# Optimization experiments

Measured on AMD Instinct MI355X. Metric: run time of the kernel, lower is better.

## Reference

```python
import math
import jax, jax.numpy as jnp
import numpy as np

D_MODEL = 1024
N_HEADS = 16
D_HEAD = D_MODEL // N_HEADS
ROPE_BASE = 10000.0
MAX_SEQ_LEN = 2048


def build_cos_sin_cache(d_head, max_seq_len, base=ROPE_BASE):
    half = d_head // 2
    i = jnp.arange(half, dtype=jnp.float32)
    theta = 1.0 / (base ** (2.0 * i / d_head))  # (half,)
    t = jnp.arange(max_seq_len, dtype=jnp.float32)
    angles = jnp.outer(t, theta)  # (T, half)
    return jnp.cos(angles), jnp.sin(angles)


def rotate_half(x):
    d = x.shape[-1]
    x1, x2 = x[..., : d // 2], x[..., d // 2 :]
    return jnp.concatenate([-x2, x1], axis=-1)


def apply_rope(x, cos_t, sin_t):
    # x: (..., T, d_head); cos_t/sin_t: (T, d_head//2)
    cos_full = jnp.concatenate([cos_t, cos_t], axis=-1)
    sin_full = jnp.concatenate([sin_t, sin_t], axis=-1)
    return x * cos_full + rotate_half(x) * sin_full


def setup_inputs() -> dict:
    key = jax.random.key(0)
    ks = jax.random.split(key, 5)
    B, T = 2, 2048
    s = 1.0 / math.sqrt(D_MODEL)
    return {
        "x": jax.random.normal(ks[0], (B, T, D_MODEL), dtype=jnp.float32),
        "Wq": jax.random.normal(ks[1], (D_MODEL, D_MODEL), dtype=jnp.float32) * s,
        "Wk": jax.random.normal(ks[2], (D_MODEL, D_MODEL), dtype=jnp.float32) * s,
        "Wv": jax.random.normal(ks[3], (D_MODEL, D_MODEL), dtype=jnp.float32) * s,
        "Wo": jax.random.normal(ks[4], (D_MODEL, D_MODEL), dtype=jnp.float32) * s,
    }


def reference(x, Wq, Wk, Wv, Wo):
    B, T, _ = x.shape
    # Linear with torch weight convention: y = x @ W.T
    q = jnp.einsum("btd,ed->bte", x, Wq)
    k = jnp.einsum("btd,ed->bte", x, Wk)
    v = jnp.einsum("btd,ed->bte", x, Wv)
    # (B, H, T, d_head)
    q = q.reshape(B, T, N_HEADS, D_HEAD).transpose(0, 2, 1, 3)
    k = k.reshape(B, T, N_HEADS, D_HEAD).transpose(0, 2, 1, 3)
    v = v.reshape(B, T, N_HEADS, D_HEAD).transpose(0, 2, 1, 3)
    cos_c, sin_c = build_cos_sin_cache(D_HEAD, MAX_SEQ_LEN)
    cos_t, sin_t = cos_c[:T], sin_c[:T]
    q = apply_rope(q, cos_t, sin_t)
    k = apply_rope(k, cos_t, sin_t)
    scale = math.sqrt(D_HEAD)
    scores = jnp.einsum("bhqd,bhkd->bhqk", q, k) / scale
    causal = jnp.triu(jnp.full((T, T), -jnp.inf, dtype=x.dtype), k=1)
    scores = scores + causal
    weights = jax.nn.softmax(scores, axis=-1)
    out = jnp.einsum("bhqk,bhkd->bhqd", weights, v)
    out = out.transpose(0, 2, 1, 3).reshape(B, T, D_MODEL)
    return jnp.einsum("btd,ed->bte", out, Wo)
```

## Files before the change

kernel.cpp:

```cpp
#include <hip/hip_runtime.h>
#include <stdint.h>
#include <math.h>

typedef __attribute__((ext_vector_type(8))) short short8;
typedef __attribute__((ext_vector_type(4))) float f32x4;
typedef __attribute__((ext_vector_type(16))) float f32x16;

#define T_SEQ 2048
#define MROWS 4096
#define LOG2E 1.44269504088896f

#define OFF_XBF   ((size_t)0)
#define OFF_WQ    ((size_t)8388608)
#define OFF_WK    ((size_t)10485760)
#define OFF_WV    ((size_t)12582912)
#define OFF_WO    ((size_t)14680064)
#define OFF_Q     ((size_t)16777216)
#define OFF_K     ((size_t)25165824)
#define OFF_VT    ((size_t)33554432)
#define OFF_ATT   ((size_t)41943040)
#define OFF_COS   ((size_t)50331648)
#define OFF_SIN   ((size_t)50593792)

__device__ __forceinline__ unsigned short f2bf(float f) {
  unsigned u = __float_as_uint(f);
  u += 0x7fffu + ((u >> 16) & 1u);
  return (unsigned short)(u >> 16);
}

__device__ __forceinline__ void gld_lds16(const void* g, void* l) {
  __builtin_amdgcn_global_load_lds(
      (__attribute__((address_space(1))) void*)(g),
      (__attribute__((address_space(3))) void*)(l), 16, 0, 0);
}

__device__ __forceinline__ unsigned cvt_pk_bf16(float lo, float hi) {
  unsigned r;
  asm("v_cvt_pk_bf16_f32 %0, %1, %2" : "=v"(r) : "v"(lo), "v"(hi));
  return r;
}

__global__ void prep_kernel(const float* x, const float* wq, const float* wk,
                            const float* wv, const float* wo, char* ws) {
  const size_t NX4 = (size_t)MROWS * 1024 / 4;
  const size_t NW4 = (size_t)1024 * 1024 / 4;
  const size_t NT = (size_t)T_SEQ * 32;
  unsigned short* xb = (unsigned short*)(ws + OFF_XBF);
  unsigned short* wqb = (unsigned short*)(ws + OFF_WQ);
  unsigned short* wkb = (unsigned short*)(ws + OFF_WK);
  unsigned short* wvb = (unsigned short*)(ws + OFF_WV);
  unsigned short* wob = (unsigned short*)(ws + OFF_WO);
  float* cosb = (float*)(ws + OFF_COS);
  float* sinb = (float*)(ws + OFF_SIN);
  size_t nvec = NX4 + 4 * NW4;
  size_t total = nvec + NT;
  for (size_t i = (size_t)blockIdx.x * blockDim.x + threadIdx.x; i < total;
       i += (size_t)gridDim.x * blockDim.x) {
    if (i < nvec) {
      const float* src;
      unsigned short* dst;
      size_t e;
      if (i < NX4) {
        src = x; dst = xb; e = i * 4;
      } else {
        size_t j = i - NX4;
        int wsel = (int)(j / NW4);
        e = (j - (size_t)wsel * NW4) * 4;
        src = wsel == 0 ? wq : wsel == 1 ? wk : wsel == 2 ? wv : wo;
        dst = wsel == 0 ? wqb : wsel == 1 ? wkb : wsel == 2 ? wvb : wob;
      }
      float4 v = *(const float4*)(src + e);
      unsigned long long p =
          (unsigned long long)f2bf(v.x) |
          ((unsigned long long)f2bf(v.y) << 16) |
          ((unsigned long long)f2bf(v.z) << 32) |
          ((unsigned long long)f2bf(v.w) << 48);
      *(unsigned long long*)(dst + e) = p;
    } else {
      size_t j = i - nvec;
      int t = (int)(j >> 5), ii = (int)(j & 31);
      double th = exp(-(double)ii * (9.210340371976184 / 32.0));
      float ang = (float)t * (float)th;
      cosb[j] = cosf(ang);
      sinb[j] = sinf(ang);
    }
  }
}

__global__ __launch_bounds__(256, 3) void gemm_qkv(
    const unsigned short* Abf, const unsigned short* Wall, unsigned short* qkout,
    unsigned short* vtout, const float* cosT, const float* sinT) {
  const int K = 1024;
  int bid0 = blockIdx.x;
  int bid = (bid0 & 7) * 96 + (bid0 >> 3);
  int bm = bid / 24, bn = bid % 24;
  int sel = bn >> 3, bnc = bn & 7;
  int tid = threadIdx.x;
  int l = tid & 63, w = tid >> 6;
  int wm = w >> 1, wn = w & 1;
  int g = l >> 4;

  __shared__ __align__(16) char ldsbuf[32768];

  auto stage = [&](int kt, int buf) {
    int base = buf * 16384;
#pragma unroll
    for (int i = 0; i < 2; ++i) {
      int p = (w * 2 + i) * 1024;
      int row = (p >> 6) + (l >> 2);
      int u = l & 3;
      const char* ga = (const char*)Abf +
          ((size_t)(bm * 128 + row) * K + (size_t)kt * 32) * 2 + u * 16;
      gld_lds16(ga, ldsbuf + base + p);
      const char* gb = (const char*)Wall +
          ((size_t)(bn * 128 + row) * K + (size_t)kt * 32) * 2 + u * 16;
      gld_lds16(gb, ldsbuf + base + 8192 + p);
    }
  };

  f32x4 acc[4][4] = {};
  stage(0, 0);
  const int nk = K / 32;
  for (int kt = 0; kt < nk; ++kt) {
    int buf = kt & 1;
    if (kt + 1 < nk) {
      stage(kt + 1, buf ^ 1);
      asm volatile("s_waitcnt vmcnt(4)" ::: "memory");
    } else {
      asm volatile("s_waitcnt vmcnt(0)" ::: "memory");
    }
    __builtin_amdgcn_s_barrier();
    __builtin_amdgcn_sched_barrier(0);
    const char* Ab = ldsbuf + buf * 16384;
    const char* Bb = Ab + 8192;
    short8 af[4], bfr[4];
#pragma unroll
    for (int m = 0; m < 4; ++m)
      af[m] = *(const short8*)(Ab + (wm * 64 + m * 16 + (l & 15)) * 64 + g * 16);
#pragma unroll
    for (int n = 0; n < 4; ++n)
      bfr[n] = *(const short8*)(Bb + (wn * 64 + n * 16 + (l & 15)) * 64 + g * 16);
#pragma unroll
    for (int m = 0; m < 4; ++m)
#pragma unroll
      for (int n = 0; n < 4; ++n)
        acc[m][n] = __builtin_amdgcn_mfma_f32_16x16x32_bf16(af[m], bfr[n],
                                                            acc[m][n], 0, 0, 0);
    __builtin_amdgcn_s_barrier();
  }

  int row0 = bm * 128 + wm * 64;
  int col0 = bnc * 128 + wn * 64;
  if (sel < 2) {
    float qscale = sel == 0 ? 0.125f * LOG2E : 1.0f;
    unsigned short* C = qkout + (size_t)sel * MROWS * 1024;
#pragma unroll
    for (int m = 0; m < 4; ++m)
#pragma unroll
      for (int n = 0; n < 2; ++n)
#pragma unroll
        for (int r = 0; r < 4; ++r) {
          int row = row0 + m * 16 + g * 4 + r;
          int t = row & (T_SEQ - 1);
          int d = n * 16 + (l & 15);
          float c = cosT[t * 32 + d], s = sinT[t * 32 + d];
          float v0 = acc[m][n][r], v1 = acc[m][n + 2][r];
          C[(size_t)row * 1024 + col0 + d] = f2bf((v0 * c - v1 * s) * qscale);
          C[(size_t)row * 1024 + col0 + d + 32] = f2bf((v1 * c + v0 * s) * qscale);
        }
  } else {
    unsigned short* C = vtout;
#pragma unroll
    for (int m = 0; m < 4; ++m) {
      int rowb = row0 + m * 16 + g * 4;
      int bb = rowb >> 11, t0 = rowb & (T_SEQ - 1);
#pragma unroll
      for (int n = 0; n < 4; ++n) {
        int e = col0 + n * 16 + (l & 15);
        unsigned long long pv =
            (unsigned long long)f2bf(acc[m][n][0]) |
            ((unsigned long long)f2bf(acc[m][n][1]) << 16) |
            ((unsigned long long)f2bf(acc[m][n][2]) << 32) |
            ((unsigned long long)f2bf(acc[m][n][3]) << 48);
        *(unsigned long long*)(C + ((size_t)bb * 1024 + e) * T_SEQ + t0) = pv;
      }
    }
  }
}

__global__ __launch_bounds__(256, 3) void gemm_wo(const unsigned short* Abf,
                                                  const unsigned short* Wbf,
                                                  float* out) {
  const int K = 1024, N = 1024;
  int bid0 = blockIdx.x;
  int bid = (bid0 & 7) * 64 + (bid0 >> 3);
  int bm = bid >> 4, bn = bid & 15;
  int tid = threadIdx.x;
  int l = tid & 63, w = tid >> 6;
  int wm = w >> 1, wn = w & 1;
  int g = l >> 4;

  __shared__ __align__(16) char ldsbuf[24576];

  auto stage = [&](int kt, int buf) {
    char* base = ldsbuf + buf * 12288;
#pragma unroll
    for (int i = 0; i < 2; ++i) {
      int pos = tid + i * 256;
      int row = pos >> 2, u = pos & 3;
      const char* ga = (const char*)Abf +
          ((size_t)(bm * 128 + row) * K + (size_t)kt * 32) * 2 + u * 16;
      gld_lds16(ga, base + row * 64 + u * 16);
    }
    {
      int row = tid >> 2, u = tid & 3;
      const char* gb = (const char*)Wbf +
          ((size_t)(bn * 64 + row) * K + (size_t)kt * 32) * 2 + u * 16;
      gld_lds16(gb, base + 8192 + row * 64 + u * 16);
    }
  };

  f32x4 acc[4][2] = {};
  stage(0, 0);
  const int nk = K / 32;
  for (int kt = 0; kt < nk; ++kt) {
    int buf = kt & 1;
    if (kt + 1 < nk) {
      stage(kt + 1, buf ^ 1);
      asm volatile("s_waitcnt vmcnt(3)" ::: "memory");
    } else {
      asm volatile("s_waitcnt vmcnt(0)" ::: "memory");
    }
    __builtin_amdgcn_s_barrier();
    __builtin_amdgcn_sched_barrier(0);
    const char* Ab = ldsbuf + buf * 12288;
    const char* Bb = Ab + 8192;
    short8 af[4], bfr[2];
#pragma unroll
    for (int m = 0; m < 4; ++m)
      af[m] = *(const short8*)(Ab + (wm * 64 + m * 16 + (l & 15)) * 64 + g * 16);
#pragma unroll
    for (int n = 0; n < 2; ++n)
      bfr[n] = *(const short8*)(Bb + (wn * 32 + n * 16 + (l & 15)) * 64 + g * 16);
#pragma unroll
    for (int m = 0; m < 4; ++m)
#pragma unroll
      for (int n = 0; n < 2; ++n)
        acc[m][n] = __builtin_amdgcn_mfma_f32_16x16x32_bf16(af[m], bfr[n],
                                                            acc[m][n], 0, 0, 0);
    __builtin_amdgcn_s_barrier();
  }

  int row0 = bm * 128 + wm * 64;
  int col0 = bn * 64 + wn * 32;
#pragma unroll
  for (int m = 0; m < 4; ++m)
#pragma unroll
    for (int n = 0; n < 2; ++n)
#pragma unroll
      for (int r = 0; r < 4; ++r)
        out[(size_t)(row0 + m * 16 + g * 4 + r) * N + col0 + n * 16 + (l & 15)] =
            acc[m][n][r];
}

__global__ __launch_bounds__(256, 2) void attn_kernel(
    const unsigned short* Qbf, const unsigned short* Kbf,
    const unsigned short* VT, unsigned short* att) {
  int bid = blockIdx.x;
  int bh = bid & 31;
  int idx = bid >> 5;
  int qt = idx < 8 ? (15 - idx) : (idx - 8);
  int b = bh >> 4, h = bh & 15;
  int ntt = 2 * qt + 2;
  int hp = ntt >> 1;

  int tid = threadIdx.x;
  int pr = tid >> 7;
  int t127 = tid & 127;
  int l = tid & 63, wv = (tid >> 6) & 1;
  int q32 = l & 31, hi = l >> 5;
  int q0 = qt * 128;
  int q0w = q0 + wv * 64;
  int myKt0 = pr ? hp : 0;
  int ntw = ((q0w + 63) >> 6) + 1 - myKt0;
  if (ntw > hp) ntw = hp;
  if (ntw < 0) ntw = 0;

  __shared__ __align__(16) char lds[2][2][16384];

  short8 qfA[4], qfB[4];
  {
    const char* qb = (const char*)Qbf +
        ((size_t)(b * T_SEQ + q0w + q32)) * 2048 + h * 128 + hi * 16;
#pragma unroll
    for (int ks = 0; ks < 4; ++ks) {
      qfA[ks] = *(const short8*)(qb + ks * 32);
      qfB[ks] = *(const short8*)(qb + 32 * 2048 + ks * 32);
    }
  }
  asm volatile("s_waitcnt vmcnt(0)" ::: "memory");

  auto stage = [&](int gt, int buf) {
    char* Kd = &lds[pr][buf][0];
    char* Vd = &lds[pr][buf][8192];
    int colb = (t127 & 7) * 16;
#pragma unroll
    for (int r = 0; r < 4; ++r) {
      int d = (t127 >> 3) + r * 16;
      int sc = colb ^ ((d & 7) << 4);
      const char* gk = (const char*)Kbf +
          ((size_t)(b * T_SEQ + gt * 64 + d)) * 2048 + h * 128 + sc;
      gld_lds16(gk, Kd + d * 128 + colb);
      const char* gv = (const char*)VT +
          ((size_t)(b * 1024 + h * 64 + d)) * 4096 + gt * 128 + sc;
      gld_lds16(gv, Vd + d * 128 + colb);
    }
  };

  f32x16 oA0 = {}, oA1 = {}, oB0 = {}, oB1 = {};
  float lA = 0.f, lB = 0.f;
  stage(myKt0, 0);
  for (int it = 0; it < hp; ++it) {
    int buf = it & 1;
    if (it + 1 < hp) {
      stage(myKt0 + it + 1, buf ^ 1);
      asm volatile("s_waitcnt vmcnt(8)" ::: "memory");
    } else {
      asm volatile("s_waitcnt vmcnt(0)" ::: "memory");
    }
    __builtin_amdgcn_s_barrier();
    __builtin_amdgcn_sched_barrier(0);
    if (it < ntw) {
      int gt = myKt0 + it;
      const char* Kl = &lds[pr][buf][0];
      const char* Vl = &lds[pr][buf][8192];

      f32x16 sA0 = {}, sA1 = {}, sB0 = {}, sB1 = {};
      __builtin_amdgcn_s_setprio(1);
#pragma unroll
      for (int ks = 0; ks < 4; ++ks) {
        int sc = (ks * 32 + hi * 16) ^ ((q32 & 7) << 4);
        short8 k0 = *(const short8*)(Kl + q32 * 128 + sc);
        short8 k1 = *(const short8*)(Kl + (q32 + 32) * 128 + sc);
        sA0 = __builtin_amdgcn_mfma_f32_32x32x16_bf16(k0, qfA[ks], sA0, 0, 0, 0);
        sA1 = __builtin_amdgcn_mfma_f32_32x32x16_bf16(k1, qfA[ks], sA1, 0, 0, 0);
        sB0 = __builtin_amdgcn_mfma_f32_32x32x16_bf16(k0, qfB[ks], sB0, 0, 0, 0);
        sB1 = __builtin_amdgcn_mfma_f32_32x32x16_bf16(k1, qfB[ks], sB1, 0, 0, 0);
      }
      __builtin_amdgcn_s_setprio(0);

      if (gt * 64 + 63 > q0w) {
        int qA = q0w + q32, qB = qA + 32;
#pragma unroll
        for (int r = 0; r < 16; ++r) {
          int kkb = gt * 64 + (r & 3) + 8 * (r >> 2) + 4 * hi;
          if (kkb > qA) sA0[r] = -1e30f;
          if (kkb + 32 > qA) sA1[r] = -1e30f;
          if (kkb > qB) sB0[r] = -1e30f;
          if (kkb + 32 > qB) sB1[r] = -1e30f;
        }
      }

      float lsA = 0.f, lsB = 0.f;
#pragma unroll
      for (int r = 0; r < 16; ++r) {
        sA0[r] = __builtin_amdgcn_exp2f(sA0[r]);
        sA1[r] = __builtin_amdgcn_exp2f(sA1[r]);
        sB0[r] = __builtin_amdgcn_exp2f(sB0[r]);
        sB1[r] = __builtin_amdgcn_exp2f(sB1[r]);
        lsA += sA0[r] + sA1[r];
        lsB += sB0[r] + sB1[r];
      }
      lA += lsA;
      lB += lsB;

      short8 pbA[4], pbB[4];
#pragma unroll
      for (int ks = 0; ks < 4; ++ks) {
        union { unsigned u[4]; short8 s8; } ua, ub;
#pragma unroll
        for (int j = 0; j < 4; ++j) {
          int bse = (ks & 1) * 8 + 2 * j;
          float a0 = (ks & 2) ? sA1[bse] : sA0[bse];
          float a1 = (ks & 2) ? sA1[bse + 1] : sA0[bse + 1];
          ua.u[j] = cvt_pk_bf16(a0, a1);
          float b0 = (ks & 2) ? sB1[bse] : sB0[bse];
          float b1 = (ks & 2) ? sB1[bse + 1] : sB0[bse + 1];
          ub.u[j] = cvt_pk_bf16(b0, b1);
        }
        pbA[ks] = ua.s8;
        pbB[ks] = ub.s8;
      }

      __builtin_amdgcn_s_setprio(1);
#pragma unroll
      for (int ks = 0; ks < 4; ++ks) {
        int sp = (q32 & 7) << 4;
        int cA = (ks * 32 + 8 * hi) ^ sp;
        int cB = (ks * 32 + 16 + 8 * hi) ^ sp;
#pragma unroll
        for (int cc = 0; cc < 2; ++cc) {
          int dv = cc * 32 + q32;
          union { unsigned long long u[2]; short8 s8; } vv;
          vv.u[0] = *(const unsigned long long*)(Vl + dv * 128 + cA);
          vv.u[1] = *(const unsigned long long*)(Vl + dv * 128 + cB);
          if (cc == 0) {
            oA0 = __builtin_amdgcn_mfma_f32_32x32x16_bf16(vv.s8, pbA[ks], oA0, 0, 0, 0);
            oB0 = __builtin_amdgcn_mfma_f32_32x32x16_bf16(vv.s8, pbB[ks], oB0, 0, 0, 0);
          } else {
            oA1 = __builtin_amdgcn_mfma_f32_32x32x16_bf16(vv.s8, pbA[ks], oA1, 0, 0, 0);
            oB1 = __builtin_amdgcn_mfma_f32_32x32x16_bf16(vv.s8, pbB[ks], oB1, 0, 0, 0);
          }
        }
      }
      __builtin_amdgcn_s_setprio(0);
    }
    __builtin_amdgcn_s_barrier();
  }

  lA += __shfl_xor(lA, 32);
  lB += __shfl_xor(lB, 32);

  float* M = (float*)(&lds[1][0][0]);
  float* Ll = (float*)(&lds[0][0][0]);
  __syncthreads();
  if (pr == 1) {
#pragma unroll
    for (int grp = 0; grp < 2; ++grp)
#pragma unroll
      for (int cc = 0; cc < 2; ++cc)
#pragma unroll
        for (int r = 0; r < 16; ++r) {
          int d = cc * 32 + (r & 3) + 8 * (r >> 2) + 4 * hi;
          float v = grp == 0 ? (cc ? oA1[r] : oA0[r]) : (cc ? oB1[r] : oB0[r]);
          M[(wv * 2 + grp) * 2048 + q32 * 64 + (d ^ (q32 & 31))] = v;
        }
    if (hi == 0) {
      Ll[wv * 128 + q32] = lA;
      Ll[wv * 128 + 64 + q32] = lB;
    }
  }
  __syncthreads();
  if (pr == 0) {
#pragma unroll
    for (int grp = 0; grp < 2; ++grp)
#pragma unroll
      for (int cc = 0; cc < 2; ++cc)
#pragma unroll
        for (int r = 0; r < 16; ++r) {
          int d = cc * 32 + (r & 3) + 8 * (r >> 2) + 4 * hi;
          float v = M[(wv * 2 + grp) * 2048 + q32 * 64 + (d ^ (q32 & 31))];
          if (grp == 0) { if (cc) oA1[r] += v; else oA0[r] += v; }
          else          { if (cc) oB1[r] += v; else oB0[r] += v; }
        }
    lA += Ll[wv * 128 + q32];
    lB += Ll[wv * 128 + 64 + q32];
  }
  __syncthreads();

  float* Ol = (float*)(&lds[0][0][0]);
  if (pr == 0) {
    float scA = 1.0f / lA;
    float scB = 1.0f / lB;
#pragma unroll
    for (int grp = 0; grp < 2; ++grp)
#pragma unroll
      for (int cc = 0; cc < 2; ++cc)
#pragma unroll
        for (int r = 0; r < 16; ++r) {
          int d = cc * 32 + (r & 3) + 8 * (r >> 2) + 4 * hi;
          float v;
          if (grp == 0) v = (cc ? oA1[r] : oA0[r]) * scA;
          else          v = (cc ? oB1[r] : oB0[r]) * scB;
          Ol[(wv * 2 + grp) * 2048 + q32 * 64 + (d ^ (q32 & 31))] = v;
        }
  }
  __syncthreads();

#pragma unroll
  for (int i = 0; i < 4; ++i) {
    int idx2 = tid + i * 256;
    int row = idx2 >> 3;
    int seg = idx2 & 7;
    int q = row & 31, rg = row >> 5;
    unsigned short tmp[8];
#pragma unroll
    for (int j = 0; j < 8; ++j) {
      int d = seg * 8 + j;
      tmp[j] = f2bf(Ol[rg * 2048 + q * 64 + (d ^ (q & 31))]);
    }
    *(unsigned long long*)(att + ((size_t)(b * T_SEQ + q0 + row)) * 1024 +
                           h * 64 + seg * 8) = *(unsigned long long*)&tmp[0];
    *(unsigned long long*)(att + ((size_t)(b * T_SEQ + q0 + row)) * 1024 +
                           h * 64 + seg * 8 + 4) = *(unsigned long long*)&tmp[4];
  }
}

extern "C" void kernel_launch(void* const* d_in, const int* in_sizes, int n_in,
                              void* d_out, int out_size, void* d_ws,
                              size_t ws_size, hipStream_t stream) {
  const float* x = (const float*)d_in[0];
  const float* Wq = (const float*)d_in[1];
  const float* Wk = (const float*)d_in[2];
  const float* Wv = (const float*)d_in[3];
  const float* Wo = (const float*)d_in[4];
  char* ws = (char*)d_ws;

  unsigned short* xb = (unsigned short*)(ws + OFF_XBF);
  unsigned short* wall = (unsigned short*)(ws + OFF_WQ);
  unsigned short* wob = (unsigned short*)(ws + OFF_WO);
  unsigned short* qbf = (unsigned short*)(ws + OFF_Q);
  unsigned short* vtb = (unsigned short*)(ws + OFF_VT);
  unsigned short* att = (unsigned short*)(ws + OFF_ATT);
  unsigned short* kbf = (unsigned short*)(ws + OFF_K);
  const float* cosT = (const float*)(ws + OFF_COS);
  const float* sinT = (const float*)(ws + OFF_SIN);

  prep_kernel<<<2048, 256, 0, stream>>>(x, Wq, Wk, Wv, Wo, ws);
  gemm_qkv<<<768, 256, 0, stream>>>(xb, wall, qbf, vtb, cosT, sinT);
  attn_kernel<<<512, 256, 0, stream>>>(qbf, kbf, vtb, att);
  gemm_wo<<<512, 256, 0, stream>>>(att, wob, (float*)d_out);
}
```

Baseline: 99.42 us.

## Double QKV GEMM K-tile to 64 with XOR-swizzled LDS layout

The QKV projection GEMM now stages 64-wide K slices per iteration instead of 32, which halves the number of barrier-synchronised main-loop iterations and doubles the LDS buffers to 64KB. It also applies an XOR swizzle on the global source address while the LDS slot stays linear, so that fragment reads with the matching XOR avoid bank conflicts. Occupancy hint drops from 3 to 2 blocks per CU because of the larger LDS footprint, which trades latency hiding for fewer syncs.

```diff
diff --git a/kernel.cpp b/kernel.cpp
--- a/kernel.cpp
+++ b/kernel.cpp
@@ -87,7 +87,7 @@
   }
 }
 
-__global__ __launch_bounds__(256, 3) void gemm_qkv(
+__global__ __launch_bounds__(256, 2) void gemm_qkv(
     const unsigned short* Abf, const unsigned short* Wall, unsigned short* qkout,
     unsigned short* vtout, const float* cosT, const float* sinT) {
   const int K = 1024;
@@ -100,52 +100,61 @@
   int wm = w >> 1, wn = w & 1;
   int g = l >> 4;
 
-  __shared__ __align__(16) char ldsbuf[32768];
+  __shared__ __align__(16) char ldsbuf[65536];
 
   auto stage = [&](int kt, int buf) {
-    int base = buf * 16384;
-#pragma unroll
-    for (int i = 0; i < 2; ++i) {
-      int p = (w * 2 + i) * 1024;
-      int row = (p >> 6) + (l >> 2);
-      int u = l & 3;
+    char* base = ldsbuf + buf * 32768;
+#pragma unroll
+    for (int i = 0; i < 4; ++i) {
+      int slot = tid + i * 256;
+      int row = slot >> 3, u = slot & 7;
+      int su = (u * 16) ^ ((row & 7) << 4);
       const char* ga = (const char*)Abf +
-          ((size_t)(bm * 128 + row) * K + (size_t)kt * 32) * 2 + u * 16;
-      gld_lds16(ga, ldsbuf + base + p);
+          ((size_t)(bm * 128 + row) * K + (size_t)kt * 64) * 2 + su;
+      gld_lds16(ga, base + row * 128 + u * 16);
       const char* gb = (const char*)Wall +
-          ((size_t)(bn * 128 + row) * K + (size_t)kt * 32) * 2 + u * 16;
-      gld_lds16(gb, ldsbuf + base + 8192 + p);
+          ((size_t)(bn * 128 + row) * K + (size_t)kt * 64) * 2 + su;
+      gld_lds16(gb, base + 16384 + row * 128 + u * 16);
     }
   };
 
   f32x4 acc[4][4] = {};
   stage(0, 0);
-  const int nk = K / 32;
+  const int nk = K / 64;
   for (int kt = 0; kt < nk; ++kt) {
     int buf = kt & 1;
     if (kt + 1 < nk) {
       stage(kt + 1, buf ^ 1);
-      asm volatile("s_waitcnt vmcnt(4)" ::: "memory");
+      asm volatile("s_waitcnt vmcnt(8)" ::: "memory");
     } else {
       asm volatile("s_waitcnt vmcnt(0)" ::: "memory");
     }
     __builtin_amdgcn_s_barrier();
     __builtin_amdgcn_sched_barrier(0);
-    const char* Ab = ldsbuf + buf * 16384;
-    const char* Bb = Ab + 8192;
-    short8 af[4], bfr[4];
-#pragma unroll
-    for (int m = 0; m < 4; ++m)
-      af[m] = *(const short8*)(Ab + (wm * 64 + m * 16 + (l & 15)) * 64 + g * 16);
-#pragma unroll
-    for (int n = 0; n < 4; ++n)
-      bfr[n] = *(const short8*)(Bb + (wn * 64 + n * 16 + (l & 15)) * 64 + g * 16);
-#pragma unroll
-    for (int m = 0; m < 4; ++m)
-#pragma unroll
-      for (int n = 0; n < 4; ++n)
-        acc[m][n] = __builtin_amdgcn_mfma_f32_16x16x32_bf16(af[m], bfr[n],
-                                                            acc[m][n], 0, 0, 0);
+    const char* Ab = ldsbuf + buf * 32768;
+    const char* Bb = Ab + 16384;
+#pragma unroll
+    for (int ks = 0; ks < 2; ++ks) {
+      short8 af[4], bfr[4];
+#pragma unroll
+      for (int m = 0; m < 4; ++m) {
+        int row = wm * 64 + m * 16 + (l & 15);
+        int col = (ks * 64 + g * 16) ^ ((row & 7) << 4);
+        af[m] = *(const short8*)(Ab + row * 128 + col);
+      }
+#pragma unroll
+      for (int n = 0; n < 4; ++n) {
+        int row = wn * 64 + n * 16 + (l & 15);
+        int col = (ks * 64 + g * 16) ^ ((row & 7) << 4);
+        bfr[n] = *(const short8*)(Bb + row * 128 + col);
+      }
+#pragma unroll
+      for (int m = 0; m < 4; ++m)
+#pragma unroll
+        for (int n = 0; n < 4; ++n)
+          acc[m][n] = __builtin_amdgcn_mfma_f32_16x16x32_bf16(af[m], bfr[n],
+                                                              acc[m][n], 0, 0, 0);
+    }
     __builtin_amdgcn_s_barrier();
   }
 
```

After: 96.65 us. 1.03x faster.
